# Kernel optimization log

Hardware: AMD Instinct MI355X
Metric: run time of the kernel (lower is better)

The kernel has to match this reference:

```python
import jax, jax.numpy as jnp
import numpy as np

B, C, H, W = 16, 64, 64, 64
HD = 128


def skew(x):
    # x: [B,C,H,W] -> [B,C,H,H+W-1], row r shifted right by r
    b, c, h, w = x.shape
    sw = h + w - 1
    xp = jnp.pad(x, ((0, 0), (0, 0), (0, 0), (0, h - 1)))
    cols = (jnp.arange(sw)[None, :] - jnp.arange(h)[:, None]) % sw  # [H,SW]
    return xp[:, :, jnp.arange(h)[:, None], cols]


def unskew(x):
    # x: [B,C,H,SW] -> [B,C,H,W]
    b, c, h, sw = x.shape
    w = sw - h + 1
    cols = jnp.arange(w)[None, :] + jnp.arange(h)[:, None]  # [H,W]
    return x[:, :, jnp.arange(h)[:, None], cols]


def setup_inputs() -> dict:
    key = jax.random.key(0)
    k1, k2, k3, k4, k5 = jax.random.split(key, 5)
    s_is = 1.0 / np.sqrt(C)
    s_ss = 1.0 / np.sqrt(HD * 2)
    return {
        "x": jax.random.normal(k1, (B, C, H, W), jnp.float32),
        "w_is": jax.random.uniform(k2, (5 * HD, C), jnp.float32, -s_is, s_is),   # 1x1 conv (mask B, k=1 => plain)
        "b_is": jax.random.uniform(k3, (5 * HD,), jnp.float32, -s_is, s_is),
        "w_ss": jax.random.uniform(k4, (5 * HD, HD, 2), jnp.float32, -s_ss, s_ss),  # Conv1d k=2
        "b_ss": jax.random.uniform(k5, (5 * HD,), jnp.float32, -s_ss, s_ss),
    }


def reference(x, w_is, b_is, w_ss, b_ss):
    hd = w_ss.shape[1]
    sk = skew(x)  # [B,C,H,SW]
    # input-to-state: 1x1 conv over skewed map
    i_s = jnp.einsum("oc,bchw->bohw", w_is, sk) + b_is[None, :, None, None]
    is_cols = jnp.moveaxis(i_s, -1, 0)  # [SW,B,5hd,H]
    w0, w1 = w_ss[:, :, 0], w_ss[:, :, 1]  # taps for h[t-1], h[t]
    bsz, h_dim = x.shape[0], x.shape[2]

    def step(carry, ic):
        h_prev, c_prev = carry
        h_sh = jnp.pad(h_prev, ((0, 0), (0, 0), (1, 0)))[:, :, :-1]
        s_s = (jnp.einsum("oi,bih->boh", w1, h_prev)
               + jnp.einsum("oi,bih->boh", w0, h_sh)
               + b_ss[None, :, None])
        gates = ic + s_s
        o, fl, fu, i, g = jnp.split(gates, 5, axis=1)
        o, fl, fu, i = map(jax.nn.sigmoid, (o, fl, fu, i))
        g = jnp.tanh(g)
        c_sh = jnp.pad(c_prev, ((0, 0), (0, 0), (1, 0)))[:, :, :-1]
        c = fl * c_prev + fu * c_sh + i * g
        h = o * jnp.tanh(c)
        return (h, c), h

    z = jnp.zeros((bsz, hd, h_dim), x.dtype)
    _, hs = jax.lax.scan(step, (z, z), is_cols)
    hs = jnp.moveaxis(hs, 0, -1)  # [B,hd,H,SW]
    return unskew(hs)
```

## Files before the change

### kernel.cpp

```cpp
#include <hip/hip_runtime.h>

typedef __attribute__((ext_vector_type(8))) short bf16x8;
typedef __attribute__((ext_vector_type(4))) float f32x4;
typedef __attribute__((ext_vector_type(4))) uint  u32x4;
typedef __attribute__((ext_vector_type(2))) uint  u32x2;

#define B_   16
#define C_   64
#define H_   64
#define W_   64
#define HD_  128
#define K_   320
#define SW_  127

#define NG    4
#define GH    32
#define NCG   64
#define TC    16
#define NT    704
#define ROWS  160
#define NKT   10
#define GPS   17

#define HSLOT  131072LL
#define CBX    524288LL
#define CNT    557056LL
#define GCNT   559104LL
#define AFB    561152LL
#define AF_N   204800LL
#define XT     765952LL
#define XT_N   4194304LL
#define WS_MIN (AFB + AF_N)
#define WS_XT  (XT + XT_N)

#define POLL_CAP (1 << 20)

__device__ __forceinline__ float sigm(float v) { return 1.f / (1.f + __expf(-v)); }
__device__ __forceinline__ float tanh_fast(float v) {
    float e = __expf(2.f * v);
    return 1.f - 2.f / (e + 1.f);
}

__device__ __forceinline__ int rload(int* p) {
    return __hip_atomic_load(p, __ATOMIC_RELAXED, __HIP_MEMORY_SCOPE_AGENT);
}
__device__ __forceinline__ void rbump(int* p) {
    __hip_atomic_fetch_add(p, 1, __ATOMIC_RELAXED, __HIP_MEMORY_SCOPE_AGENT);
}
__device__ __forceinline__ void wait_ge(int* p, int tgt) {
    int guard = 0;
    while (rload(p) < tgt) { if (++guard > POLL_CAP) break; }
    __atomic_signal_fence(__ATOMIC_ACQUIRE);
}

__device__ __forceinline__ void stu_nw(uint* p, uint v) {
    asm volatile("global_store_dword %0, %1, off sc1" :: "v"(p), "v"(v) : "memory");
}
__device__ __forceinline__ void st2_nw(uint* p, u32x2 v) {
    asm volatile("global_store_dwordx2 %0, %1, off sc1" :: "v"(p), "v"(v) : "memory");
}

__device__ __forceinline__ void poll1(const uint* p, uint want, u32x4& A) {
    int guard = 0;
    while (true) {
        u32x4 a;
        asm volatile("global_load_dwordx4 %0, %1, off sc1\n\ts_waitcnt vmcnt(0)"
                     : "=&v"(a) : "v"(p) : "memory");
        uint m = a[0] & a[1] & a[2] & a[3];
        uint o = a[0] | a[1] | a[2] | a[3];
        bool ok = want ? ((m & 1u) != 0u) : ((o & 1u) == 0u);
        if (ok || ++guard > POLL_CAP) { A = a; return; }
    }
}

__device__ __forceinline__ uint bf16hi(uint u) { return (u + 0x7FFFu + ((u >> 16) & 1u)) >> 16; }
__device__ __forceinline__ uint2 splitbf(float v) {
    uint uh = bf16hi(__float_as_uint(v));
    float rl = v - __uint_as_float(uh << 16);
    uint ul = bf16hi(__float_as_uint(rl));
    return make_uint2(uh, ul);
}

__global__ void lstm_prep(const float* __restrict__ w_is,
                          const float* __restrict__ w_ss,
                          float* __restrict__ ws, long long n_ws)
{
    const long long stride = (long long)gridDim.x * blockDim.x;
    const long long t0 = (long long)blockIdx.x * blockDim.x + threadIdx.x;
    uint* wsu = (uint*)ws;

    for (long long i = t0; i < 524288LL + 32768LL; i += stride) {
        long long a = (i < 524288LL) ? i : (CBX + (i - 524288LL));
        stu_nw(wsu + a, 0x00000001u);
    }
    for (long long i = CNT + t0; i < CNT + 4096; i += stride)
        stu_nw(wsu + i, 0u);

    if (n_ws >= WS_MIN) {
        ushort* af = (ushort*)(ws + AFB);
        for (long long e = t0; e < AF_N; e += stride) {
            int idx   = (int)e;
            int chunk = idx >> 9;
            int lane  = (idx >> 3) & 63;
            int jj    = idx & 7;
            int g  = chunk / (10 * NKT);
            int rm = chunk % (10 * NKT);
            int rt = rm / NKT, kt = rm % NKT;
            int m = lane & 15, quad = lane >> 4;
            int r = rt * 16 + m;
            int q = r >> 5, hl = r & 31;
            int o = q * HD_ + g * GH + hl;
            int k = kt * 32 + quad * 8 + jj;
            float v;
            if (k < C_)            v = w_is[o * C_ + k];
            else if (k < C_ + HD_) v = w_ss[(o * HD_ + (k - C_)) * 2 + 1];
            else                   v = w_ss[(o * HD_ + (k - C_ - HD_)) * 2 + 0];
            uint uh = bf16hi(__float_as_uint(v));
            float rl = v - __uint_as_float(uh << 16);
            uint ul = bf16hi(__float_as_uint(rl));
            int base = chunk * 1024 + lane * 16 + jj;
            af[base]     = (ushort)uh;
            af[base + 8] = (ushort)ul;
        }
    }
}

__global__ void lstm_xpose(const float* __restrict__ x, float* __restrict__ ws)
{
    __shared__ float L[64 * 65];
    const int b = blockIdx.x >> 6, hr = blockIdx.x & 63;
    const int tid = threadIdx.x;
    #pragma unroll
    for (int it = 0; it < 16; ++it) {
        int c = it * 4 + (tid >> 6), w = tid & 63;
        L[c * 65 + w] = x[(((size_t)b * C_ + c) * H_ + hr) * W_ + w];
    }
    __syncthreads();
    float* xt = ws + XT;
    #pragma unroll
    for (int it = 0; it < 16; ++it) {
        int w = it * 4 + (tid >> 6), c = tid & 63;
        xt[(((size_t)b * H_ + hr) * W_ + w) * C_ + c] = L[c * 65 + w];
    }
}

__global__ void __launch_bounds__(NT, 2) lstm_persist(
    const float* __restrict__ x,
    const float* __restrict__ ws_c,
    const float* __restrict__ b_is,
    const float* __restrict__ b_ss,
    float* __restrict__ out,
    float* __restrict__ ws,
    int use_xt)
{
    __shared__ uint  Bf[NKT * 576];
    __shared__ float Gp[ROWS * GPS];
    __shared__ float Cs[2][17 * GH];
    __shared__ float bias_s[ROWS];

    const int tid = threadIdx.x;
    const int cgp = blockIdx.x >> 2;
    const int g   = blockIdx.x & 3;
    const int n0  = cgp * TC;
    const int inb  = (n0 & 63) != 0;
    const int hasr = ((n0 + TC) & 63) != 0;

    uint* hring = (uint*)ws;
    uint* cring = (uint*)(ws + CBX);
    int*  gcntp = (int*)(ws + GCNT);
    const float* xt = ws_c + XT;
    const uint4* afq = (const uint4*)(ws_c + AFB);

    if (tid < ROWS) {
        int q = tid >> 5, hl = tid & 31;
        int o = q * HD_ + g * GH + hl;
        bias_s[tid] = b_is[o] + b_ss[o];
    }
    if (tid < 17 * GH) Cs[0][tid] = 0.f;
    if (tid >= 544 && tid < 544 + GH) Cs[1][tid - 544] = 0.f;

    const int lane = tid & 63;
    const int wv   = tid >> 6;
    const int quad = lane >> 4;
    const int colc = lane & 15;
    uint* bfr = &Bf[lane * 8 + ((lane >> 2) << 2)];

    const int cp  = tid >> 5;
    const int ch  = tid & 31;
    const int pq  = (ch >> 1) & 3;
    const int pj0 = (ch & 1) * 4;
    const int kta = 2 + (ch >> 3);
    const int laneA = pq * 16 + ((cp >= 1) ? (cp - 1) : 0);
    const int laneB = pq * 16 + ((cp <= 15) ? cp : 0);
    uint* bfA = &Bf[laneA * 8 + ((laneA >> 2) << 2) + kta * 576 + (pj0 >> 1)];
    uint* bfB = &Bf[laneB * 8 + ((laneB >> 2) << 2) + (kta + 4) * 576 + (pj0 >> 1)];
    const uint* hbase = hring + (size_t)(n0 - 1 + cp) * 128 + ch * 4;
    const int pskip = (cp == 0 && !inb);

    const int xi = tid - 544;
    const int xkt = xi >> 6, xl = xi & 63;
    const int xq = xl >> 4, xcolc = xl & 15;
    const int xc0 = xkt * 32 + xq * 8;
    const int xn = n0 + xcolc, xb = xn >> 6, xhr = xn & 63;
    uint* bfX = &Bf[xl * 8 + ((xl >> 2) << 2) + xkt * 576];

    const int ci = tid - 672;

    bf16x8 Ahr[NKT], Alr[NKT];
    if (wv < 10) {
        const uint4* ap0 = afq + (size_t)((g * 10 + wv) * NKT) * 128 + lane * 2;
        #pragma unroll
        for (int kt = 0; kt < NKT; ++kt) {
            uint4 ha = ap0[kt * 128];
            Ahr[kt] = *(bf16x8*)&ha;
            asm volatile("" : "+v"(Ahr[kt]));
            uint4 la = ap0[kt * 128 + 1];
            Alr[kt] = *(bf16x8*)&la;
            asm volatile("" : "+v"(Alr[kt]));
        }
    }

    __syncthreads();

    for (int j = 0; j < SW_; ++j) {
        const uint want = ((j - 1) >> 2) & 1u;
        const uint wtag = (j >> 2) & 1u;

        if (tid < 544) {
            u32x4 a = {0, 0, 0, 0};
            if (j > 0 && !pskip)
                poll1(hbase + (size_t)((j - 1) & 3) * HSLOT, want, a);
            uint2 e0 = splitbf(__uint_as_float(a[0]));
            uint2 e1 = splitbf(__uint_as_float(a[1]));
            uint2 e2 = splitbf(__uint_as_float(a[2]));
            uint2 e3 = splitbf(__uint_as_float(a[3]));
            u32x2 hp = {e0.x | (e1.x << 16), e2.x | (e3.x << 16)};
            u32x2 lp = {e0.y | (e1.y << 16), e2.y | (e3.y << 16)};
            if (cp >= 1)  { *(u32x2*)bfA = hp; *(u32x2*)(bfA + 4) = lp; }
            if (cp <= 15) { *(u32x2*)bfB = hp; *(u32x2*)(bfB + 4) = lp; }
        } else if (tid < 672) {
            float xv[8];
            int w = j - xhr;
            if ((unsigned)w < (unsigned)W_) {
                if (use_xt) {
                    const float* xp = xt + (((size_t)xb * H_ + xhr) * W_ + w) * C_ + xc0;
                    f32x4 va = *(const f32x4*)xp, vb = *(const f32x4*)(xp + 4);
                    #pragma unroll
                    for (int r = 0; r < 4; ++r) { xv[r] = va[r]; xv[4 + r] = vb[r]; }
                } else {
                    #pragma unroll
                    for (int r = 0; r < 8; ++r)
                        xv[r] = x[(((size_t)xb * C_ + xc0 + r) * H_ + xhr) * W_ + w];
                }
            } else {
                #pragma unroll
                for (int r = 0; r < 8; ++r) xv[r] = 0.f;
            }
            uint hw[4], lw[4];
            #pragma unroll
            for (int p = 0; p < 4; ++p) {
                uint2 e0 = splitbf(xv[2 * p]), e1 = splitbf(xv[2 * p + 1]);
                hw[p] = e0.x | (e1.x << 16);
                lw[p] = e0.y | (e1.y << 16);
            }
            *(uint4*)bfX       = make_uint4(hw[0], hw[1], hw[2], hw[3]);
            *(uint4*)(bfX + 4) = make_uint4(lw[0], lw[1], lw[2], lw[3]);
        } else if (ci >= 0 && ci < 8) {
            if (inb && j > 0) {
                u32x4 cv;
                const uint* cpx = cring +
                    (((size_t)((j - 1) & 3) * NCG + (cgp - 1)) * NG + g) * GH + ci * 4;
                poll1(cpx, want, cv);
                #pragma unroll
                for (int r = 0; r < 4; ++r)
                    Cs[j & 1][ci * 4 + r] = __uint_as_float(cv[r]);
            }
        } else if (ci == 8) {
            if (j >= 4 && hasr) wait_ge(gcntp + (cgp + 1) * 32, 4 * (j - 2));
        }
        __syncthreads();
        if (tid == 0) rbump(gcntp + cgp * 32);

        if (wv < 10) {
            f32x4 acc0 = {0.f, 0.f, 0.f, 0.f};
            f32x4 acc1 = {0.f, 0.f, 0.f, 0.f};
            __builtin_amdgcn_s_setprio(1);
            #pragma unroll
            for (int kt = 0; kt < NKT; kt += 2) {
                const uint* bp0 = bfr + kt * 576;
                uint4 hb0 = *(const uint4*)bp0;
                uint4 lb0 = *(const uint4*)(bp0 + 4);
                const uint* bp1 = bfr + (kt + 1) * 576;
                uint4 hb1 = *(const uint4*)bp1;
                uint4 lb1 = *(const uint4*)(bp1 + 4);
                bf16x8 Bh0 = *(bf16x8*)&hb0, Bl0 = *(bf16x8*)&lb0;
                bf16x8 Bh1 = *(bf16x8*)&hb1, Bl1 = *(bf16x8*)&lb1;
                acc0 = __builtin_amdgcn_mfma_f32_16x16x32_bf16(Ahr[kt],     Bh0, acc0, 0, 0, 0);
                acc1 = __builtin_amdgcn_mfma_f32_16x16x32_bf16(Ahr[kt + 1], Bh1, acc1, 0, 0, 0);
                acc0 = __builtin_amdgcn_mfma_f32_16x16x32_bf16(Ahr[kt],     Bl0, acc0, 0, 0, 0);
                acc1 = __builtin_amdgcn_mfma_f32_16x16x32_bf16(Ahr[kt + 1], Bl1, acc1, 0, 0, 0);
                acc0 = __builtin_amdgcn_mfma_f32_16x16x32_bf16(Alr[kt],     Bh0, acc0, 0, 0, 0);
                acc1 = __builtin_amdgcn_mfma_f32_16x16x32_bf16(Alr[kt + 1], Bh1, acc1, 0, 0, 0);
                acc0 = __builtin_amdgcn_mfma_f32_16x16x32_bf16(Alr[kt],     Bl0, acc0, 0, 0, 0);
                acc1 = __builtin_amdgcn_mfma_f32_16x16x32_bf16(Alr[kt + 1], Bl1, acc1, 0, 0, 0);
            }
            __builtin_amdgcn_s_setprio(0);
            #pragma unroll
            for (int r = 0; r < 4; ++r)
                Gp[(wv * 16 + quad * 4 + r) * GPS + colc] = acc0[r] + acc1[r];
        }
        __syncthreads();

        if (tid < GH * TC) {
            const int hl = tid & 31, col = tid >> 5;
            int n = n0 + col, b = n >> 6, hr = n & 63;
            float go  = Gp[(0 * GH + hl) * GPS + col] + bias_s[0 * GH + hl];
            float gfl = Gp[(1 * GH + hl) * GPS + col] + bias_s[1 * GH + hl];
            float gfu = Gp[(2 * GH + hl) * GPS + col] + bias_s[2 * GH + hl];
            float gi  = Gp[(3 * GH + hl) * GPS + col] + bias_s[3 * GH + hl];
            float gg  = Gp[(4 * GH + hl) * GPS + col] + bias_s[4 * GH + hl];
            float so = sigm(go), sfl = sigm(gfl), sfu = sigm(gfu), si = sigm(gi);
            float tg = tanh_fast(gg);
            float cp_ = Cs[j & 1][(col + 1) * GH + hl];
            float cs = Cs[j & 1][col * GH + hl];
            float cv = sfl * cp_ + sfu * cs + si * tg;
            float hv = so * tanh_fast(cv);
            Cs[(j + 1) & 1][(col + 1) * GH + hl] = cv;

            uint pk = (__float_as_uint(hv) & ~1u) | wtag;
            uint other = (uint)__shfl_xor((int)pk, 1);
            if (!(hl & 1)) {
                u32x2 pv = {pk, other};
                st2_nw(hring + (size_t)(j & 3) * HSLOT + (size_t)n * 128 + g * GH + (hl & ~1), pv);
            }
            if (col == TC - 1) {
                uint cpk = (__float_as_uint(cv) & ~1u) | wtag;
                stu_nw(cring + (((size_t)(j & 3) * NCG + cgp) * NG + g) * GH + hl, cpk);
            }
            int w = j - hr;
            if ((unsigned)w < (unsigned)W_)
                out[(((size_t)b * HD_ + g * GH + hl) * H_ + hr) * W_ + w] = hv;
        }
    }
}

extern "C" void kernel_launch(void* const* d_in, const int* in_sizes, int n_in,
                              void* d_out, int out_size, void* d_ws, size_t ws_size,
                              hipStream_t stream)
{
    const float* x    = (const float*)d_in[0];
    const float* w_is = (const float*)d_in[1];
    const float* b_is = (const float*)d_in[2];
    const float* w_ss = (const float*)d_in[3];
    const float* b_ss = (const float*)d_in[4];
    float* out = (float*)d_out;
    float* ws  = (float*)d_ws;

    const long long n_ws = (long long)(ws_size / 4);
    const int use_xt = (n_ws >= WS_XT) ? 1 : 0;

    hipLaunchKernelGGL(lstm_prep, dim3(1024), dim3(256), 0, stream,
                       w_is, w_ss, ws, n_ws);
    if (use_xt)
        hipLaunchKernelGGL(lstm_xpose, dim3(B_ * H_), dim3(256), 0, stream, x, ws);

    hipLaunchKernelGGL(lstm_persist, dim3(NG * NCG), dim3(NT), 0, stream,
                       x, ws, b_is, b_ss, out, ws, use_xt);
}
```

Measured before the change: 492.4 us.

## Fuse input transpose into prep kernel and stage output through coalesced scratch transpose

The x transpose is merged into the prep kernel by doubling its grid, which removes one launch. The persistent LSTM kernel now writes h values into a scratch buffer laid out [n][w][hd], and a new kernel transposes that buffer into the [B,HD,H,W] output. The aim is to replace strided scattered output stores in the critical recurrent loop with contiguous ones. In exchange it adds an extra read and write pass over the output, another launch, and a larger workspace requirement. The prep grid also grows, so the strided weight loops now spread across twice as many threads.

```diff
diff --git a/kernel.cpp b/kernel.cpp
--- a/kernel.cpp
+++ b/kernel.cpp
@@ -30,8 +30,11 @@
 #define AF_N   204800LL
 #define XT     765952LL
 #define XT_N   4194304LL
+#define OSC    (XT + XT_N)
+#define OSC_N  8388608LL
 #define WS_MIN (AFB + AF_N)
 #define WS_XT  (XT + XT_N)
+#define WS_OSC (OSC + OSC_N)
 
 #define POLL_CAP (1 << 20)
 
@@ -81,10 +84,12 @@
     return make_uint2(uh, ul);
 }
 
-__global__ void lstm_prep(const float* __restrict__ w_is,
+__global__ void lstm_prep(const float* __restrict__ x,
+                          const float* __restrict__ w_is,
                           const float* __restrict__ w_ss,
-                          float* __restrict__ ws, long long n_ws)
+                          float* __restrict__ ws, long long n_ws, int use_xt)
 {
+    __shared__ float L[64 * 65];
     const long long stride = (long long)gridDim.x * blockDim.x;
     const long long t0 = (long long)blockIdx.x * blockDim.x + threadIdx.x;
     uint* wsu = (uint*)ws;
@@ -123,24 +128,44 @@
             af[base + 8] = (ushort)ul;
         }
     }
-}
-
-__global__ void lstm_xpose(const float* __restrict__ x, float* __restrict__ ws)
+
+    if (use_xt && blockIdx.x >= 1024) {
+        const int bb = blockIdx.x - 1024;
+        const int b = bb >> 6, hr = bb & 63;
+        const int tid = threadIdx.x;
+        #pragma unroll
+        for (int it = 0; it < 16; ++it) {
+            int c = it * 4 + (tid >> 6), w = tid & 63;
+            L[c * 65 + w] = x[(((size_t)b * C_ + c) * H_ + hr) * W_ + w];
+        }
+        __syncthreads();
+        float* xt = ws + XT;
+        #pragma unroll
+        for (int it = 0; it < 16; ++it) {
+            int w = it * 4 + (tid >> 6), c = tid & 63;
+            xt[(((size_t)b * H_ + hr) * W_ + w) * C_ + c] = L[c * 65 + w];
+        }
+    }
+}
+
+__global__ void lstm_oxpose(const float* __restrict__ ws, float* __restrict__ out)
 {
-    __shared__ float L[64 * 65];
-    const int b = blockIdx.x >> 6, hr = blockIdx.x & 63;
+    __shared__ float L[64 * 129];
+    const int n = blockIdx.x, b = n >> 6, hr = n & 63;
+    const float* osc = ws + OSC + (size_t)n * 64 * 128;
     const int tid = threadIdx.x;
     #pragma unroll
-    for (int it = 0; it < 16; ++it) {
-        int c = it * 4 + (tid >> 6), w = tid & 63;
-        L[c * 65 + w] = x[(((size_t)b * C_ + c) * H_ + hr) * W_ + w];
+    for (int it = 0; it < 32; ++it) {
+        int e = it * 256 + tid;
+        int w = e >> 7, hd = e & 127;
+        L[w * 129 + hd] = osc[e];
     }
     __syncthreads();
-    float* xt = ws + XT;
     #pragma unroll
-    for (int it = 0; it < 16; ++it) {
-        int w = it * 4 + (tid >> 6), c = tid & 63;
-        xt[(((size_t)b * H_ + hr) * W_ + w) * C_ + c] = L[c * 65 + w];
+    for (int it = 0; it < 32; ++it) {
+        int e = it * 256 + tid;
+        int hd = e >> 6, w = e & 63;
+        out[(((size_t)b * HD_ + hd) * H_ + hr) * W_ + w] = L[w * 129 + hd];
     }
 }
 
@@ -151,7 +176,7 @@
     const float* __restrict__ b_ss,
     float* __restrict__ out,
     float* __restrict__ ws,
-    int use_xt)
+    int use_xt, int use_osc)
 {
     __shared__ uint  Bf[NKT * 576];
     __shared__ float Gp[ROWS * GPS];
@@ -168,6 +193,7 @@
     uint* hring = (uint*)ws;
     uint* cring = (uint*)(ws + CBX);
     int*  gcntp = (int*)(ws + GCNT);
+    float* osc = ws + OSC;
     const float* xt = ws_c + XT;
     const uint4* afq = (const uint4*)(ws_c + AFB);
 
@@ -338,8 +364,12 @@
                 stu_nw(cring + (((size_t)(j & 3) * NCG + cgp) * NG + g) * GH + hl, cpk);
             }
             int w = j - hr;
-            if ((unsigned)w < (unsigned)W_)
-                out[(((size_t)b * HD_ + g * GH + hl) * H_ + hr) * W_ + w] = hv;
+            if ((unsigned)w < (unsigned)W_) {
+                if (use_osc)
+                    osc[((size_t)n * 64 + w) * 128 + g * GH + hl] = hv;
+                else
+                    out[(((size_t)b * HD_ + g * GH + hl) * H_ + hr) * W_ + w] = hv;
+            }
         }
     }
 }
@@ -357,13 +387,15 @@
     float* ws  = (float*)d_ws;
 
     const long long n_ws = (long long)(ws_size / 4);
-    const int use_xt = (n_ws >= WS_XT) ? 1 : 0;
-
-    hipLaunchKernelGGL(lstm_prep, dim3(1024), dim3(256), 0, stream,
-                       w_is, w_ss, ws, n_ws);
-    if (use_xt)
-        hipLaunchKernelGGL(lstm_xpose, dim3(B_ * H_), dim3(256), 0, stream, x, ws);
+    const int use_xt  = (n_ws >= WS_XT)  ? 1 : 0;
+    const int use_osc = (n_ws >= WS_OSC) ? 1 : 0;
+
+    hipLaunchKernelGGL(lstm_prep, dim3(2048), dim3(256), 0, stream,
+                       x, w_is, w_ss, ws, n_ws, use_xt);
 
     hipLaunchKernelGGL(lstm_persist, dim3(NG * NCG), dim3(NT), 0, stream,
-                       x, ws, b_is, b_ss, out, ws, use_xt);
-}
+                       x, ws, b_is, b_ss, out, ws, use_xt, use_osc);
+
+    if (use_osc)
+        hipLaunchKernelGGL(lstm_oxpose, dim3(1024), dim3(256), 0, stream, ws, out);
+}
```

After: 483.4 us. Within noise of the previous version (-1.8%).
